# Performance work log

Hardware: AMD Instinct MI355X
Metric: run time of the kernel (lower is better)

The kernel has to match this reference:

```python
import jax, jax.numpy as jnp
import numpy as np

IN_FEATURES = 4096
OUT_FEATURES = 4096
TOKENS = 8192
QMAX = 127.0


def setup_inputs() -> dict:
    key = jax.random.key(0)
    k1, k2, k3, k4 = jax.random.split(key, 4)
    x = jax.random.normal(k1, (TOKENS, IN_FEATURES), dtype=jnp.float32)
    # int8 quantized weights in [-127, 127]
    Wq = jax.random.randint(k2, (OUT_FEATURES, IN_FEATURES), -127, 128, dtype=jnp.int32).astype(jnp.int8)
    # per-row absmax scales (positive)
    row_scales = jax.random.uniform(k3, (OUT_FEATURES,), dtype=jnp.float32, minval=0.01, maxval=1.0)
    bias_param = jax.random.normal(k4, (OUT_FEATURES,), dtype=jnp.float32)
    return {"x": x, "Wq": Wq, "row_scales": row_scales, "bias_param": bias_param}


def reference(x, Wq, row_scales, bias_param):
    # rowwise dequant: W[o, i] = Wq[o, i] * row_scales[o] / 127
    W_dequant = Wq.astype(x.dtype) * (row_scales.astype(x.dtype) / QMAX)[:, None]  # [O, I]
    Y = jnp.matmul(x, W_dequant.T)  # [T, O]
    return Y + bias_param.astype(x.dtype)
```

## Files before the change

kernel.cpp:

```cpp
#include <hip/hip_runtime.h>

#define M_TOK 8192
#define N_OUT 4096
#define K_IN  4096

#define AS1 __attribute__((address_space(1)))
#define AS3 __attribute__((address_space(3)))

typedef __attribute__((ext_vector_type(4))) int i32x4;
typedef __attribute__((ext_vector_type(16))) int i32x16;

template <int OFF>
__device__ __forceinline__ i32x4 dsri(unsigned addr) {
    i32x4 r;
    asm volatile("ds_read_b128 %0, %1 offset:%2" : "=v"(r) : "v"(addr), "n"(OFF));
    return r;
}


__global__ __launch_bounds__(256) void quant_x_kernel(
    const float* __restrict__ x, signed char* __restrict__ xq,
    float* __restrict__ tok_scale)
{
    const int row = blockIdx.x;
    const float4* xr = reinterpret_cast<const float4*>(x + (size_t)row * K_IN);
    const int t = threadIdx.x;
    float4 v[4];
    float m = 0.f;
#pragma unroll
    for (int i = 0; i < 4; ++i) {
        v[i] = xr[t + 256 * i];
        m = fmaxf(m, fmaxf(fmaxf(fabsf(v[i].x), fabsf(v[i].y)),
                           fmaxf(fabsf(v[i].z), fabsf(v[i].w))));
    }
#pragma unroll
    for (int off = 32; off >= 1; off >>= 1)
        m = fmaxf(m, __shfl_xor(m, off, 64));
    __shared__ float wmax[4];
    if ((t & 63) == 0) wmax[t >> 6] = m;
    __syncthreads();
    m = fmaxf(fmaxf(wmax[0], wmax[1]), fmaxf(wmax[2], wmax[3]));
    if (t == 0) tok_scale[row] = m * (1.0f / 127.0f);
    const float inv = (m > 0.f) ? (127.0f / m) : 0.f;
    int* xqi = reinterpret_cast<int*>(xq + (size_t)row * K_IN);
#pragma unroll
    for (int i = 0; i < 4; ++i) {
        const int q0 = __float2int_rn(v[i].x * inv) & 255;
        const int q1 = __float2int_rn(v[i].y * inv) & 255;
        const int q2 = __float2int_rn(v[i].z * inv) & 255;
        const int q3 = __float2int_rn(v[i].w * inv) & 255;
        xqi[t + 256 * i] = q0 | (q1 << 8) | (q2 << 16) | (q3 << 24);
    }
}


__global__ __launch_bounds__(256) void retile_x_kernel(
    const signed char* __restrict__ xq8, signed char* __restrict__ xqF)
{
    __shared__ __align__(16) char lds[32768];
    const int t = threadIdx.x;
    const int rb = blockIdx.x >> 2;
    const int kc = blockIdx.x & 3;

    const size_t srcBase = (size_t)rb * 32 * K_IN + (size_t)kc * 1024;
#pragma unroll
    for (int j = 0; j < 8; ++j) {
        const int u = j * 256 + t;
        const int row = u >> 6, gc = u & 63;
        const i32x4 v = *reinterpret_cast<const i32x4*>(
            xq8 + srcBase + (size_t)row * K_IN + gc * 16);
        *reinterpret_cast<i32x4*>(
            lds + ((row * 64 + (gc ^ (row & 7))) * 16)) = v;
    }
    __syncthreads();

    const int l = t & 63;
    const int W = t >> 6;
    const int row = l & 31;
    const int hi = l >> 5;
    i32x4* dst0 = reinterpret_cast<i32x4*>(xqF) +
                  ((size_t)rb * 128 + kc * 32) * 64 + l;
#pragma unroll
    for (int i = 0; i < 8; ++i) {
        const int kfl = W * 8 + i;
        const int gc = (kfl * 2 + hi) ^ (row & 7);
        const i32x4 v = *reinterpret_cast<const i32x4*>(
            lds + ((row * 64 + gc) * 16));
        dst0[(size_t)kfl * 64] = v;
    }
}


__global__ __launch_bounds__(256) void pack_w_frag_kernel(
    const int* __restrict__ wq, signed char* __restrict__ wqF)
{
    const int t = threadIdx.x;
    const int l = t & 63;
    const int W = t >> 6;
    const int rb = blockIdx.x >> 3;
    const int pc = blockIdx.x & 7;
    const int r = rb * 32 + (l & 31);
    const int4* wr4 = reinterpret_cast<const int4*>(wq) + (size_t)r * 1024;
    i32x4* outF = reinterpret_cast<i32x4*>(wqF) + (size_t)rb * 128 * 64 + l;
#pragma unroll
    for (int q = 0; q < 4; ++q) {
        const int f = W + 4 * (pc * 4 + q);
        const int c4 = f * 8 + (l >> 5) * 4;
        i32x4 o;
#pragma unroll
        for (int j = 0; j < 4; ++j) {
            const int4 a = wr4[c4 + j];
            o[j] = (a.x & 255) | ((a.y & 255) << 8) | ((a.z & 255) << 16) | ((a.w & 255) << 24);
        }
        outF[(size_t)f * 64] = o;
    }
}


#define NKT 128
#define SLOTA 8192
#define SLOTB 8192

#define MFMA(a, b, c) c = __builtin_amdgcn_mfma_i32_32x32x32_i8(a, b, c, 0, 0, 0)

#define RD6(P, aA, bA)                          \
    P##_B0 = dsri<0>(bA);                       \
    P##_B1 = dsri<1024>(bA);                    \
    P##_A0 = dsri<0>(aA);                       \
    P##_A1 = dsri<1024>(aA);                    \
    P##_A2 = dsri<2048>(aA);                    \
    P##_A3 = dsri<3072>(aA);

#define CL4a(P)                                               \
    MFMA(P##_A0, P##_B0, acc00); MFMA(P##_A0, P##_B1, acc01); \
    MFMA(P##_A1, P##_B0, acc10); MFMA(P##_A1, P##_B1, acc11);

#define CL4b(P)                                               \
    MFMA(P##_A2, P##_B0, acc20); MFMA(P##_A2, P##_B1, acc21); \
    MFMA(P##_A3, P##_B0, acc30); MFMA(P##_A3, P##_B1, acc31);

#define GBODY(T, C, N, DO_STAGE)                                          \
    {                                                                     \
        asm volatile("s_waitcnt lgkmcnt(2)" ::: "memory");                \
        __builtin_amdgcn_sched_barrier(0);                                \
        __builtin_amdgcn_s_setprio(1);                                    \
        CL4a(C)                                                           \
        __builtin_amdgcn_s_setprio(0);                                    \
        __builtin_amdgcn_sched_barrier(0);                                \
        const unsigned aN_ = aBase + (unsigned)((((T) + 1) & 3) * SLOTA); \
        const unsigned bN_ = bBase + (unsigned)((((T) + 1) & 3) * SLOTB); \
        RD6(N, aN_, bN_)                                                  \
        if (DO_STAGE) stageAB((T) + 3);                                   \
        asm volatile("s_waitcnt lgkmcnt(6)" ::: "memory");                \
        __builtin_amdgcn_sched_barrier(0);                                \
        __builtin_amdgcn_s_setprio(1);                                    \
        CL4b(C)                                                           \
        __builtin_amdgcn_s_setprio(0);                                    \
        __builtin_amdgcn_sched_barrier(0);                                \
        if (DO_STAGE) { asm volatile("s_waitcnt vmcnt(2)" ::: "memory"); }\
        else          { asm volatile("s_waitcnt vmcnt(0)" ::: "memory"); }\
        __builtin_amdgcn_sched_barrier(0);                                \
        __builtin_amdgcn_s_barrier();                                     \
        __builtin_amdgcn_sched_barrier(0);                                \
    }

#define GFINAL(C)                                                         \
    {                                                                     \
        asm volatile("s_waitcnt lgkmcnt(2)" ::: "memory");                \
        __builtin_amdgcn_sched_barrier(0);                                \
        __builtin_amdgcn_s_setprio(1);                                    \
        CL4a(C)                                                           \
        __builtin_amdgcn_s_setprio(0);                                    \
        asm volatile("s_waitcnt lgkmcnt(0)" ::: "memory");                \
        __builtin_amdgcn_sched_barrier(0);                                \
        __builtin_amdgcn_s_setprio(1);                                    \
        CL4b(C)                                                           \
        __builtin_amdgcn_s_setprio(0);                                    \
        __builtin_amdgcn_sched_barrier(0);                                \
    }

__global__ __launch_bounds__(512, 2) void qgemm_i8c_kernel(
    const signed char* __restrict__ xqF,
    const signed char* __restrict__ wqF,
    const float* __restrict__ tok_scale,
    const float* __restrict__ row_scales,
    const float* __restrict__ bias,
    float* __restrict__ out)
{
    __shared__ __align__(16) char smem[65536];

    const int tid = threadIdx.x;
    const int l = tid & 63;
    const int w = tid >> 6;
    const int wr = w >> 2;
    const int wc = w & 3;

    const int bid = blockIdx.x;
    const int swz = (bid & 7) * 64 + (bid >> 3);
    const int bm = swz >> 4;
    const int bn = swz & 15;

    const signed char* aS = xqF + ((size_t)(bm * 8 + w) * 128) * 1024 + (size_t)l * 16;
    const signed char* bS = wqF + ((size_t)(bn * 8 + w) * 128) * 1024 + (size_t)l * 16;
    char* aDst = smem + w * 1024;
    char* bDst = smem + 32768 + w * 1024;

    auto stageAB = [&](int tt) {
        __builtin_amdgcn_global_load_lds(
            (const AS1 void*)(aS + (size_t)tt * 1024),
            (AS3 void*)(aDst + (tt & 3) * SLOTA), 16, 0, 0);
        __builtin_amdgcn_global_load_lds(
            (const AS1 void*)(bS + (size_t)tt * 1024),
            (AS3 void*)(bDst + (tt & 3) * SLOTB), 16, 0, 0);
    };

    const unsigned sbase = (unsigned)(uintptr_t)(AS3 char*)smem;
    const unsigned aBase = sbase + (unsigned)(wr * 4096 + l * 16);
    const unsigned bBase = sbase + 32768u + (unsigned)(wc * 2048 + l * 16);

    i32x16 acc00 = {0}, acc01 = {0}, acc10 = {0}, acc11 = {0};
    i32x16 acc20 = {0}, acc21 = {0}, acc30 = {0}, acc31 = {0};

    i32x4 X_A0, X_A1, X_A2, X_A3, X_B0, X_B1;
    i32x4 Y_A0, Y_A1, Y_A2, Y_A3, Y_B0, Y_B1;

    stageAB(0); stageAB(1); stageAB(2);
    asm volatile("s_waitcnt vmcnt(2)" ::: "memory");
    __builtin_amdgcn_sched_barrier(0);
    __builtin_amdgcn_s_barrier();
    __builtin_amdgcn_sched_barrier(0);
    RD6(X, aBase, bBase)

    for (int t = 0; t < 126; t += 2) {
        GBODY(t,     X, Y, (t + 3 < NKT));
        GBODY(t + 1, Y, X, (t + 4 < NKT));
    }
    GBODY(126, X, Y, false);
    GFINAL(Y)

    const int cl = l & 31;
    const int rg4 = (l >> 5) * 4;
    const int gcol0 = bn * 256 + wc * 64;
    const float* tsrow = tok_scale + bm * 256 + wr * 128;
    float cs[2], bb[2];
#pragma unroll
    for (int nb = 0; nb < 2; ++nb) {
        const int col = gcol0 + nb * 32 + cl;
        cs[nb] = row_scales[col] * (1.0f / 127.0f);
        bb[nb] = bias[col];
    }
    const i32x16* accs[4][2] = {{&acc00, &acc01}, {&acc10, &acc11},
                                {&acc20, &acc21}, {&acc30, &acc31}};
#pragma unroll
    for (int mb = 0; mb < 4; ++mb) {
#pragma unroll
        for (int reg = 0; reg < 16; ++reg) {
            const int rloc = wr * 128 + mb * 32 + (reg & 3) + 8 * (reg >> 2) + rg4;
            const float tsv = tsrow[mb * 32 + (reg & 3) + 8 * (reg >> 2) + rg4];
            float* orow = out + (size_t)(bm * 256 + rloc) * N_OUT + gcol0 + cl;
#pragma unroll
            for (int nb = 0; nb < 2; ++nb) {
                const int a = (*accs[mb][nb])[reg];
                orow[nb * 32] = (float)a * tsv * cs[nb] + bb[nb];
            }
        }
    }
}


extern "C" void kernel_launch(void* const* d_in, const int* in_sizes, int n_in,
                              void* d_out, int out_size, void* d_ws, size_t ws_size,
                              hipStream_t stream) {
    const float* x = (const float*)d_in[0];
    const int* wq = (const int*)d_in[1];
    const float* row_scales = (const float*)d_in[2];
    const float* bias = (const float*)d_in[3];
    float* out = (float*)d_out;

    signed char* xq8 = (signed char*)d_ws;
    signed char* xqF = xq8 + (size_t)M_TOK * K_IN;
    signed char* wqF = xqF + (size_t)M_TOK * K_IN;
    float* tok_scale = (float*)(wqF + (size_t)N_OUT * K_IN);
    (void)ws_size;

    quant_x_kernel<<<M_TOK, 256, 0, stream>>>(x, xq8, tok_scale);
    pack_w_frag_kernel<<<1024, 256, 0, stream>>>(wq, wqF);
    retile_x_kernel<<<1024, 256, 0, stream>>>(xq8, xqF);

    const int nblocks = (M_TOK / 256) * (N_OUT / 256);
    qgemm_i8c_kernel<<<nblocks, 512, 0, stream>>>(
        xqF, wqF, tok_scale, row_scales, bias, out);
}
```

Baseline: 193.5 us.

## Shrink GEMM block to 256x128 tile with 4 waves per workgroup

The int8 GEMM workgroup changes from 8 waves on a 256x256 output tile to 4 waves on a 256x128 tile. Each wave now stages two A fragments and one B fragment per k-step. The B LDS slot size is halved and total LDS drops to 48KB. The grid doubles and the vmcnt waits are retuned for three outstanding loads per stage. The aim is more resident blocks and better load balancing, at the cost of lower B reuse per block and more global traffic for A.

New measurement: 197.7 us. 1.02x slower.

```diff
diff --git a/kernel.cpp b/kernel.cpp
--- a/kernel.cpp
+++ b/kernel.cpp
@@ -119,7 +119,7 @@
 
 #define NKT 128
 #define SLOTA 8192
-#define SLOTB 8192
+#define SLOTB 4096
 
 #define MFMA(a, b, c) c = __builtin_amdgcn_mfma_i32_32x32x32_i8(a, b, c, 0, 0, 0)
 
@@ -139,7 +139,7 @@
     MFMA(P##_A2, P##_B0, acc20); MFMA(P##_A2, P##_B1, acc21); \
     MFMA(P##_A3, P##_B0, acc30); MFMA(P##_A3, P##_B1, acc31);
 
-#define GBODY(T, C, N, DO_STAGE)                                          \
+#define GBODY(T, C, N, DO_STAGE, VM)                                      \
     {                                                                     \
         asm volatile("s_waitcnt lgkmcnt(2)" ::: "memory");                \
         __builtin_amdgcn_sched_barrier(0);                                \
@@ -157,8 +157,7 @@
         CL4b(C)                                                           \
         __builtin_amdgcn_s_setprio(0);                                    \
         __builtin_amdgcn_sched_barrier(0);                                \
-        if (DO_STAGE) { asm volatile("s_waitcnt vmcnt(2)" ::: "memory"); }\
-        else          { asm volatile("s_waitcnt vmcnt(0)" ::: "memory"); }\
+        asm volatile("s_waitcnt vmcnt(" #VM ")" ::: "memory");            \
         __builtin_amdgcn_sched_barrier(0);                                \
         __builtin_amdgcn_s_barrier();                                     \
         __builtin_amdgcn_sched_barrier(0);                                \
@@ -179,7 +178,7 @@
         __builtin_amdgcn_sched_barrier(0);                                \
     }
 
-__global__ __launch_bounds__(512, 2) void qgemm_i8c_kernel(
+__global__ __launch_bounds__(256, 2) void qgemm_i8w4_kernel(
     const signed char* __restrict__ xqF,
     const signed char* __restrict__ wqF,
     const float* __restrict__ tok_scale,
@@ -187,31 +186,36 @@
     const float* __restrict__ bias,
     float* __restrict__ out)
 {
-    __shared__ __align__(16) char smem[65536];
+    __shared__ __align__(16) char smem[49152];
 
     const int tid = threadIdx.x;
     const int l = tid & 63;
     const int w = tid >> 6;
-    const int wr = w >> 2;
-    const int wc = w & 3;
+    const int wr = w >> 1;
+    const int wc = w & 1;
 
     const int bid = blockIdx.x;
-    const int swz = (bid & 7) * 64 + (bid >> 3);
-    const int bm = swz >> 4;
-    const int bn = swz & 15;
-
-    const signed char* aS = xqF + ((size_t)(bm * 8 + w) * 128) * 1024 + (size_t)l * 16;
-    const signed char* bS = wqF + ((size_t)(bn * 8 + w) * 128) * 1024 + (size_t)l * 16;
-    char* aDst = smem + w * 1024;
+    const int swz = (bid & 7) * 128 + (bid >> 3);
+    const int bm = swz >> 5;
+    const int bn = swz & 31;
+
+    const signed char* aS0 = xqF + ((size_t)(bm * 8 + 2 * w) * 128) * 1024 + (size_t)l * 16;
+    const signed char* bS  = wqF + ((size_t)(bn * 4 + w) * 128) * 1024 + (size_t)l * 16;
+    char* aDst = smem + w * 2048;
     char* bDst = smem + 32768 + w * 1024;
 
     auto stageAB = [&](int tt) {
+        const unsigned sa = (tt & 3) * SLOTA;
+        const unsigned sb = (tt & 3) * SLOTB;
         __builtin_amdgcn_global_load_lds(
-            (const AS1 void*)(aS + (size_t)tt * 1024),
-            (AS3 void*)(aDst + (tt & 3) * SLOTA), 16, 0, 0);
+            (const AS1 void*)(aS0 + (size_t)tt * 1024),
+            (AS3 void*)(aDst + sa), 16, 0, 0);
+        __builtin_amdgcn_global_load_lds(
+            (const AS1 void*)(aS0 + 131072 + (size_t)tt * 1024),
+            (AS3 void*)(aDst + sa + 1024), 16, 0, 0);
         __builtin_amdgcn_global_load_lds(
             (const AS1 void*)(bS + (size_t)tt * 1024),
-            (AS3 void*)(bDst + (tt & 3) * SLOTB), 16, 0, 0);
+            (AS3 void*)(bDst + sb), 16, 0, 0);
     };
 
     const unsigned sbase = (unsigned)(uintptr_t)(AS3 char*)smem;
@@ -225,22 +229,24 @@
     i32x4 Y_A0, Y_A1, Y_A2, Y_A3, Y_B0, Y_B1;
 
     stageAB(0); stageAB(1); stageAB(2);
-    asm volatile("s_waitcnt vmcnt(2)" ::: "memory");
+    asm volatile("s_waitcnt vmcnt(3)" ::: "memory");
     __builtin_amdgcn_sched_barrier(0);
     __builtin_amdgcn_s_barrier();
     __builtin_amdgcn_sched_barrier(0);
     RD6(X, aBase, bBase)
 
-    for (int t = 0; t < 126; t += 2) {
-        GBODY(t,     X, Y, (t + 3 < NKT));
-        GBODY(t + 1, Y, X, (t + 4 < NKT));
-    }
-    GBODY(126, X, Y, false);
+    for (int t = 0; t < 124; t += 2) {
+        GBODY(t,     X, Y, true, 3);
+        GBODY(t + 1, Y, X, true, 3);
+    }
+    GBODY(124, X, Y, true, 3);
+    GBODY(125, Y, X, false, 0);
+    GBODY(126, X, Y, false, 0);
     GFINAL(Y)
 
     const int cl = l & 31;
     const int rg4 = (l >> 5) * 4;
-    const int gcol0 = bn * 256 + wc * 64;
+    const int gcol0 = bn * 128 + wc * 64;
     const float* tsrow = tok_scale + bm * 256 + wr * 128;
     float cs[2], bb[2];
 #pragma unroll
@@ -255,9 +261,9 @@
     for (int mb = 0; mb < 4; ++mb) {
 #pragma unroll
         for (int reg = 0; reg < 16; ++reg) {
-            const int rloc = wr * 128 + mb * 32 + (reg & 3) + 8 * (reg >> 2) + rg4;
-            const float tsv = tsrow[mb * 32 + (reg & 3) + 8 * (reg >> 2) + rg4];
-            float* orow = out + (size_t)(bm * 256 + rloc) * N_OUT + gcol0 + cl;
+            const int rl = mb * 32 + (reg & 3) + 8 * (reg >> 2) + rg4;
+            const float tsv = tsrow[rl];
+            float* orow = out + (size_t)(bm * 256 + wr * 128 + rl) * N_OUT + gcol0 + cl;
 #pragma unroll
             for (int nb = 0; nb < 2; ++nb) {
                 const int a = (*accs[mb][nb])[reg];
@@ -287,7 +293,7 @@
     pack_w_frag_kernel<<<1024, 256, 0, stream>>>(wq, wqF);
     retile_x_kernel<<<1024, 256, 0, stream>>>(xq8, xqF);
 
-    const int nblocks = (M_TOK / 256) * (N_OUT / 256);
-    qgemm_i8c_kernel<<<nblocks, 512, 0, stream>>>(
+    const int nblocks = (M_TOK / 256) * (N_OUT / 128);
+    qgemm_i8w4_kernel<<<nblocks, 256, 0, stream>>>(
         xqF, wqF, tok_scale, row_scales, bias, out);
 }
```

## Load B fragments directly from global into registers, bypassing LDS

Applied to the files above, without the earlier changes.

The weight (B) operand is no longer staged through shared memory. Each wave now reads its pre-packed MFMA fragments straight from global memory into registers, using a triple-buffered register rotation two k-steps ahead. The A operand stays on the LDS path. This halves LDS use and drops the LDS reads for B, at the cost of extra register pressure and B traffic that each wave row fetches redundantly; the vmcnt accounting also becomes more intricate.

After: 200.2 us. 3.5% more time.

```diff
diff --git a/kernel.cpp b/kernel.cpp
--- a/kernel.cpp
+++ b/kernel.cpp
@@ -119,67 +119,71 @@
 
 #define NKT 128
 #define SLOTA 8192
-#define SLOTB 8192
 
 #define MFMA(a, b, c) c = __builtin_amdgcn_mfma_i32_32x32x32_i8(a, b, c, 0, 0, 0)
 
-#define RD6(P, aA, bA)                          \
-    P##_B0 = dsri<0>(bA);                       \
-    P##_B1 = dsri<1024>(bA);                    \
+#define RD4(P, aA)                              \
     P##_A0 = dsri<0>(aA);                       \
     P##_A1 = dsri<1024>(aA);                    \
     P##_A2 = dsri<2048>(aA);                    \
     P##_A3 = dsri<3072>(aA);
 
-#define CL4a(P)                                               \
-    MFMA(P##_A0, P##_B0, acc00); MFMA(P##_A0, P##_B1, acc01); \
-    MFMA(P##_A1, P##_B0, acc10); MFMA(P##_A1, P##_B1, acc11);
-
-#define CL4b(P)                                               \
-    MFMA(P##_A2, P##_B0, acc20); MFMA(P##_A2, P##_B1, acc21); \
-    MFMA(P##_A3, P##_B0, acc30); MFMA(P##_A3, P##_B1, acc31);
-
-#define GBODY(T, C, N, DO_STAGE)                                          \
+#define RDB(P, TT)                                       \
+    P##_B0 = bSrc[(size_t)(TT) * 64];                    \
+    P##_B1 = bSrc[(size_t)(128 + (TT)) * 64];
+
+#define CL4a(PA, PB)                                                \
+    MFMA(PA##_A0, PB##_B0, acc00); MFMA(PA##_A0, PB##_B1, acc01);   \
+    MFMA(PA##_A1, PB##_B0, acc10); MFMA(PA##_A1, PB##_B1, acc11);
+
+#define CL4b(PA, PB)                                                \
+    MFMA(PA##_A2, PB##_B0, acc20); MFMA(PA##_A2, PB##_B1, acc21);   \
+    MFMA(PA##_A3, PB##_B0, acc30); MFMA(PA##_A3, PB##_B1, acc31);
+
+#define GBODY(T, CA, NA, CB, NB, DO_G, DO_B, VME, VMB)                    \
     {                                                                     \
+        asm volatile("s_waitcnt vmcnt(" #VME ")" ::: "memory");           \
+        __builtin_amdgcn_sched_barrier(0);                                \
         asm volatile("s_waitcnt lgkmcnt(2)" ::: "memory");                \
         __builtin_amdgcn_sched_barrier(0);                                \
         __builtin_amdgcn_s_setprio(1);                                    \
-        CL4a(C)                                                           \
+        CL4a(CA, CB)                                                      \
         __builtin_amdgcn_s_setprio(0);                                    \
         __builtin_amdgcn_sched_barrier(0);                                \
         const unsigned aN_ = aBase + (unsigned)((((T) + 1) & 3) * SLOTA); \
-        const unsigned bN_ = bBase + (unsigned)((((T) + 1) & 3) * SLOTB); \
-        RD6(N, aN_, bN_)                                                  \
-        if (DO_STAGE) stageAB((T) + 3);                                   \
-        asm volatile("s_waitcnt lgkmcnt(6)" ::: "memory");                \
+        RD4(NA, aN_)                                                      \
+        if (DO_G) stageA((T) + 3);                                        \
+        if (DO_B) { RDB(NB, (T) + 2) }                                    \
+        asm volatile("s_waitcnt lgkmcnt(4)" ::: "memory");                \
         __builtin_amdgcn_sched_barrier(0);                                \
         __builtin_amdgcn_s_setprio(1);                                    \
-        CL4b(C)                                                           \
+        CL4b(CA, CB)                                                      \
         __builtin_amdgcn_s_setprio(0);                                    \
         __builtin_amdgcn_sched_barrier(0);                                \
-        if (DO_STAGE) { asm volatile("s_waitcnt vmcnt(2)" ::: "memory"); }\
-        else          { asm volatile("s_waitcnt vmcnt(0)" ::: "memory"); }\
+        asm volatile("s_waitcnt vmcnt(" #VMB ")" ::: "memory");           \
         __builtin_amdgcn_sched_barrier(0);                                \
         __builtin_amdgcn_s_barrier();                                     \
         __builtin_amdgcn_sched_barrier(0);                                \
     }
 
-#define GFINAL(C)                                                         \
+#define GFINAL(CA, CB)                                                    \
     {                                                                     \
+        asm volatile("s_waitcnt vmcnt(0)" ::: "memory");                  \
+        __builtin_amdgcn_sched_barrier(0);                                \
         asm volatile("s_waitcnt lgkmcnt(2)" ::: "memory");                \
         __builtin_amdgcn_sched_barrier(0);                                \
         __builtin_amdgcn_s_setprio(1);                                    \
-        CL4a(C)                                                           \
+        CL4a(CA, CB)                                                      \
         __builtin_amdgcn_s_setprio(0);                                    \
         asm volatile("s_waitcnt lgkmcnt(0)" ::: "memory");                \
         __builtin_amdgcn_sched_barrier(0);                                \
         __builtin_amdgcn_s_setprio(1);                                    \
-        CL4b(C)                                                           \
+        CL4b(CA, CB)                                                      \
         __builtin_amdgcn_s_setprio(0);                                    \
         __builtin_amdgcn_sched_barrier(0);                                \
     }
 
-__global__ __launch_bounds__(512, 2) void qgemm_i8c_kernel(
+__global__ __launch_bounds__(512, 2) void qgemm_i8bd_kernel(
     const signed char* __restrict__ xqF,
     const signed char* __restrict__ wqF,
     const float* __restrict__ tok_scale,
@@ -187,7 +191,7 @@
     const float* __restrict__ bias,
     float* __restrict__ out)
 {
-    __shared__ __align__(16) char smem[65536];
+    __shared__ __align__(16) char smem[4 * SLOTA];
 
     const int tid = threadIdx.x;
     const int l = tid & 63;
@@ -201,42 +205,52 @@
     const int bn = swz & 15;
 
     const signed char* aS = xqF + ((size_t)(bm * 8 + w) * 128) * 1024 + (size_t)l * 16;
-    const signed char* bS = wqF + ((size_t)(bn * 8 + w) * 128) * 1024 + (size_t)l * 16;
     char* aDst = smem + w * 1024;
-    char* bDst = smem + 32768 + w * 1024;
-
-    auto stageAB = [&](int tt) {
+
+    auto stageA = [&](int tt) {
         __builtin_amdgcn_global_load_lds(
             (const AS1 void*)(aS + (size_t)tt * 1024),
             (AS3 void*)(aDst + (tt & 3) * SLOTA), 16, 0, 0);
-        __builtin_amdgcn_global_load_lds(
-            (const AS1 void*)(bS + (size_t)tt * 1024),
-            (AS3 void*)(bDst + (tt & 3) * SLOTB), 16, 0, 0);
     };
+
+    const i32x4* bSrc = reinterpret_cast<const i32x4*>(
+        wqF + ((size_t)(bn * 8 + wc * 2) * 128) * 1024) + l;
 
     const unsigned sbase = (unsigned)(uintptr_t)(AS3 char*)smem;
     const unsigned aBase = sbase + (unsigned)(wr * 4096 + l * 16);
-    const unsigned bBase = sbase + 32768u + (unsigned)(wc * 2048 + l * 16);
 
     i32x16 acc00 = {0}, acc01 = {0}, acc10 = {0}, acc11 = {0};
     i32x16 acc20 = {0}, acc21 = {0}, acc30 = {0}, acc31 = {0};
 
-    i32x4 X_A0, X_A1, X_A2, X_A3, X_B0, X_B1;
-    i32x4 Y_A0, Y_A1, Y_A2, Y_A3, Y_B0, Y_B1;
-
-    stageAB(0); stageAB(1); stageAB(2);
+    i32x4 X_A0, X_A1, X_A2, X_A3;
+    i32x4 Y_A0, Y_A1, Y_A2, Y_A3;
+    i32x4 R_B0, R_B1, S_B0, S_B1, U_B0, U_B1;
+
+    stageA(0); stageA(1); stageA(2);
+    RDB(R, 0)
+    RDB(S, 1)
     asm volatile("s_waitcnt vmcnt(2)" ::: "memory");
     __builtin_amdgcn_sched_barrier(0);
     __builtin_amdgcn_s_barrier();
     __builtin_amdgcn_sched_barrier(0);
-    RD6(X, aBase, bBase)
-
-    for (int t = 0; t < 126; t += 2) {
-        GBODY(t,     X, Y, (t + 3 < NKT));
-        GBODY(t + 1, Y, X, (t + 4 < NKT));
-    }
-    GBODY(126, X, Y, false);
-    GFINAL(Y)
+    RD4(X, aBase)
+
+    for (int t = 0; t < 120; t += 6) {
+        GBODY(t + 0, X, Y, R, U, true, true, 3, 5);
+        GBODY(t + 1, Y, X, S, R, true, true, 3, 5);
+        GBODY(t + 2, X, Y, U, S, true, true, 3, 5);
+        GBODY(t + 3, Y, X, R, U, true, true, 3, 5);
+        GBODY(t + 4, X, Y, S, R, true, true, 3, 5);
+        GBODY(t + 5, Y, X, U, S, true, true, 3, 5);
+    }
+    GBODY(120, X, Y, R, U, true,  true,  3, 5);
+    GBODY(121, Y, X, S, R, true,  true,  3, 5);
+    GBODY(122, X, Y, U, S, true,  true,  3, 5);
+    GBODY(123, Y, X, R, U, true,  true,  3, 5);
+    GBODY(124, X, Y, S, R, true,  true,  3, 5);
+    GBODY(125, Y, X, U, S, false, true,  3, 4);
+    GBODY(126, X, Y, R, R, false, false, 2, 2);
+    GFINAL(Y, S)
 
     const int cl = l & 31;
     const int rg4 = (l >> 5) * 4;
@@ -255,9 +269,9 @@
     for (int mb = 0; mb < 4; ++mb) {
 #pragma unroll
         for (int reg = 0; reg < 16; ++reg) {
-            const int rloc = wr * 128 + mb * 32 + (reg & 3) + 8 * (reg >> 2) + rg4;
-            const float tsv = tsrow[mb * 32 + (reg & 3) + 8 * (reg >> 2) + rg4];
-            float* orow = out + (size_t)(bm * 256 + rloc) * N_OUT + gcol0 + cl;
+            const int rl = mb * 32 + (reg & 3) + 8 * (reg >> 2) + rg4;
+            const float tsv = tsrow[rl];
+            float* orow = out + (size_t)(bm * 256 + wr * 128 + rl) * N_OUT + gcol0 + cl;
 #pragma unroll
             for (int nb = 0; nb < 2; ++nb) {
                 const int a = (*accs[mb][nb])[reg];
@@ -288,6 +302,6 @@
     retile_x_kernel<<<1024, 256, 0, stream>>>(xq8, xqF);
 
     const int nblocks = (M_TOK / 256) * (N_OUT / 256);
-    qgemm_i8c_kernel<<<nblocks, 512, 0, stream>>>(
+    qgemm_i8bd_kernel<<<nblocks, 512, 0, stream>>>(
         xqF, wqF, tok_scale, row_scales, bias, out);
 }
```
